# Performance work log

Hardware: AMD Instinct MI355X
Metric: run time of the kernel (lower is better)

## Reference

```python
import jax, jax.numpy as jnp
import numpy as np

B, N, DF = 8, 4096, 768
K1, K2, DS = 8, 2, 128
KVQ, H, ITERS = 128, 1, 3
DH = KVQ // H
EPS_SA = 1e-8
SCALE = DH ** -0.5


def layer_norm(x, g, b, eps=1e-5):
    m = jnp.mean(x, axis=-1, keepdims=True)
    v = jnp.var(x, axis=-1, keepdims=True)
    return (x - m) / jnp.sqrt(v + eps) * g + b


def gru_cell(x, h, Wih, Whh, bih, bhh):
    gi = x @ Wih.T + bih
    gh = h @ Whh.T + bhh
    ir, iz, inn = jnp.split(gi, 3, axis=-1)
    hr, hz, hn = jnp.split(gh, 3, axis=-1)
    r = jax.nn.sigmoid(ir + hr)
    z = jax.nn.sigmoid(iz + hz)
    n = jnp.tanh(inn + r * hn)
    return (1.0 - z) * n + z * h


def setup_inputs() -> dict:
    key = jax.random.key(0)
    ks = jax.random.split(key, 24)
    s = 0.02
    f32 = jnp.float32
    return {
        'tokens': jax.random.normal(ks[0], (B, N, DF), f32),
        'parent_slots': jax.random.normal(ks[1], (B, K1, DS), f32),
        'parent_masks': jax.random.uniform(ks[2], (B, K1, N), f32),
        'eps_noise': jax.random.normal(ks[3], (B, K1, K2, DS), f32),
        'ln_in_g': jnp.ones((DF,), f32), 'ln_in_b': jnp.zeros((DF,), f32),
        'ln_s_g': jnp.ones((DS,), f32), 'ln_s_b': jnp.zeros((DS,), f32),
        'Wq': jax.random.normal(ks[4], (KVQ, DS), f32) * s,
        'Wk': jax.random.normal(ks[5], (KVQ, DF), f32) * s,
        'Wv': jax.random.normal(ks[6], (KVQ, DF), f32) * s,
        'gru_Wih': jax.random.normal(ks[7], (3 * DS, KVQ), f32) * s,
        'gru_Whh': jax.random.normal(ks[8], (3 * DS, DS), f32) * s,
        'gru_bih': jnp.zeros((3 * DS,), f32),
        'gru_bhh': jnp.zeros((3 * DS,), f32),
        'mlp_ln_g': jnp.ones((DS,), f32), 'mlp_ln_b': jnp.zeros((DS,), f32),
        'mlp_W1': jax.random.normal(ks[9], (4 * DS, DS), f32) * s,
        'mlp_b1': jnp.zeros((4 * DS,), f32),
        'mlp_W2': jax.random.normal(ks[10], (DS, 4 * DS), f32) * s,
        'mlp_b2': jnp.zeros((DS,), f32),
    }


def reference(tokens, parent_slots, parent_masks, eps_noise,
              ln_in_g, ln_in_b, ln_s_g, ln_s_b, Wq, Wk, Wv,
              gru_Wih, gru_Whh, gru_bih, gru_bhh,
              mlp_ln_g, mlp_ln_b, mlp_W1, mlp_b1, mlp_W2, mlp_b2):
    BK = B * K1
    # parent-mask gating (all parents vectorized, folded into batch)
    denom = jnp.mean(parent_masks, axis=-1, keepdims=True)          # [B,K1,1]
    safe = (denom > 1e-6).astype(tokens.dtype)
    w_scaled = safe * (parent_masks / (denom + 1e-6)) + (1.0 - safe)  # [B,K1,N]
    tg = (tokens[:, None, :, :] * w_scaled[..., None]).reshape(BK, N, DF)
    slots = (parent_slots[:, :, None, :] + 0.01 * eps_noise).reshape(BK, K2, DS)

    inp = layer_norm(tg, ln_in_g, ln_in_b)
    k = (inp @ Wk.T).reshape(BK, N, H, DH)
    v = (inp @ Wv.T).reshape(BK, N, H, DH)

    attn_bw = None
    for _ in range(ITERS):
        slots_prev = slots
        sn = layer_norm(slots, ln_s_g, ln_s_b)
        q = (sn @ Wq.T).reshape(BK, K2, H, DH)
        dots = jnp.einsum('bihd,bjhd->bihj', q, k) * SCALE          # [BK,K2,H,N]
        attn = jax.nn.softmax(dots, axis=1) + EPS_SA                # softmax over slots
        attn_bw = attn
        attn_w = attn / jnp.sum(attn, axis=-1, keepdims=True)
        updates = jnp.einsum('bjhd,bihj->bihd', v, attn_w).reshape(BK * K2, KVQ)
        slots = gru_cell(updates, slots_prev.reshape(BK * K2, DS),
                         gru_Wih, gru_Whh, gru_bih, gru_bhh).reshape(BK, K2, DS)
        h = layer_norm(slots, mlp_ln_g, mlp_ln_b)
        slots = jax.nn.gelu(h @ mlp_W1.T + mlp_b1, approximate=False) @ mlp_W2.T + mlp_b2

    attn_out = jnp.mean(attn_bw, axis=2)                            # [BK,K2,N]
    child_objects = slots.reshape(B, K1 * K2, DS)
    child_gating = (attn_out.reshape(B, K1, K2, N) * parent_masks[:, :, None, :]).reshape(B, K1 * K2, N)
    return child_objects, child_gating
```

## Files before the change

kernel.cpp:

```cpp
#include <hip/hip_runtime.h>
#include <math.h>

#define SCALE_ 0.08838834764831843f

typedef __attribute__((ext_vector_type(8))) short bf16x8;
typedef __attribute__((ext_vector_type(4))) float f32x4;

static const size_t OFF_VAR   = 0;
static const size_t OFF_DENOM = 32768;
static const size_t OFF_GSUM  = 32832;
static const size_t OFF_BIAS  = 33088;
static const size_t OFF_QKB   = 33344;
static const size_t OFF_SSUM  = 33472;
static const size_t OFF_SLOTS = 33600;
static const size_t OFF_Q     = 49984;
static const size_t OFF_WQT   = 66368;
static const size_t OFF_WQBF  = 82752;
static const size_t OFF_WIHBF = 90944;
static const size_t OFF_WHHBF = 115520;
static const size_t OFF_W1BF  = 140096;
static const size_t OFF_WM2BF = 172864;
static const size_t OFF_WKVBF = 205632;
static const size_t OFF_UPART = 303936;
static const size_t OFF_KV    = 828224;

__device__ __forceinline__ float wred64(float v) {
#pragma unroll
  for (int off = 32; off > 0; off >>= 1) v += __shfl_xor(v, off, 64);
  return v;
}

__device__ __forceinline__ float2 bred128(float a, float b, float* red4, int t) {
  float ra = wred64(a), rb = wred64(b);
  int wid = t >> 6;
  if ((t & 63) == 0) { red4[wid] = ra; red4[2 + wid] = rb; }
  __syncthreads();
  float2 o; o.x = red4[0] + red4[1]; o.y = red4[2] + red4[3];
  __syncthreads();
  return o;
}

__device__ __forceinline__ unsigned short f2bf(float f) {
  unsigned u = __float_as_uint(f);
  unsigned r = (u + 0x7fffu + ((u >> 16) & 1u)) >> 16;
  return (unsigned short)r;
}

__device__ __forceinline__ unsigned pack2(float a, float b) {
  return (unsigned)f2bf(a) | ((unsigned)f2bf(b) << 16);
}

__global__ __launch_bounds__(64) void prep_w_k(
    const float* __restrict__ Wk, const float* __restrict__ Wv,
    const float* __restrict__ g, const float* __restrict__ bb,
    unsigned short* __restrict__ wkv, float* __restrict__ gsum,
    float* __restrict__ biasArr)
{
  int j = blockIdx.x, lane = threadIdx.x;
  const float* w = (j < 128) ? (Wk + (size_t)j*768) : (Wv + (size_t)(j-128)*768);
  float gs = 0.f, bs = 0.f;
#pragma unroll
  for (int s = 0; s < 12; ++s) {
    int dd = lane + s*64;
    float wv = w[dd], gv = g[dd];
    gs += gv*wv; bs += bb[dd]*wv;
    wkv[(size_t)j*768 + dd] = f2bf(wv*gv);
  }
  gs = wred64(gs); bs = wred64(bs);
  if (lane == 0) { gsum[j] = gs; biasArr[j] = bs; }
}

__global__ __launch_bounds__(256) void prep_bf_k(
    const float* __restrict__ Wq, const float* __restrict__ Wih,
    const float* __restrict__ Whh, const float* __restrict__ W1,
    const float* __restrict__ W2,
    float* __restrict__ WqT, unsigned short* __restrict__ Wqbf,
    unsigned short* __restrict__ Wihbf, unsigned short* __restrict__ Whhbf,
    unsigned short* __restrict__ W1bf, unsigned short* __restrict__ Wm2bf)
{
  int bi = blockIdx.x, t = threadIdx.x;
  if (bi < 64) {
    int idx = bi*256 + t;
    int r = idx >> 7, c = idx & 127;
    WqT[(size_t)c*128 + r] = Wq[idx];
    Wqbf[idx] = f2bf(Wq[idx]);
    return;
  }
  const float* src; unsigned short* dst; int idx;
  if (bi < 256)      { src = Wih; dst = Wihbf; idx = (bi-64)*256 + t; }
  else if (bi < 448) { src = Whh; dst = Whhbf; idx = (bi-256)*256 + t; }
  else if (bi < 704) { src = W1;  dst = W1bf;  idx = (bi-448)*256 + t; }
  else               { src = W2;  dst = Wm2bf; idx = (bi-704)*256 + t; }
  dst[idx] = f2bf(src[idx]);
}

__global__ __launch_bounds__(256) void denom_k(
    const float* __restrict__ pm, float* __restrict__ denomArr)
{
  __shared__ float red4[4];
  int bk = blockIdx.x, t = threadIdx.x;
  float s = 0.f;
#pragma unroll
  for (int k = 0; k < 16; ++k) s += pm[bk*4096 + t + k*256];
  s = wred64(s);
  if ((t & 63) == 0) red4[t >> 6] = s;
  __syncthreads();
  if (t == 0) denomArr[bk] = (red4[0]+red4[1]+red4[2]+red4[3])*(1.f/4096.f);
}

__global__ __launch_bounds__(256) void gemm_kv_k(
    const float* __restrict__ tokens, const unsigned short* __restrict__ wkv,
    const float* __restrict__ gsum, float* __restrict__ KV,
    float* __restrict__ varArr)
{
  __shared__ unsigned short As[128*64];
  __shared__ unsigned short Bs[128*64];
  int bi = blockIdx.x;
  int jb = bi & 1, rb = bi >> 1;
  int r0 = rb*128, j0 = jb*128;
  int t = threadIdx.x;
  int w = t >> 6, lane = t & 63;
  int j4 = t & 15, rowb = t >> 4;
  int m0w = (w >> 1)*64, n0w = (w & 1)*64;
  int lm = lane & 15, lq = lane >> 4;

  f32x4 acc[4][4];
#pragma unroll
  for (int a = 0; a < 4; ++a)
#pragma unroll
    for (int c = 0; c < 4; ++c) acc[a][c] = f32x4{0.f, 0.f, 0.f, 0.f};

  float s1[8], s2[8];
#pragma unroll
  for (int s = 0; s < 8; ++s) { s1[s] = 0.f; s2[s] = 0.f; }

  for (int k0 = 0; k0 < 768; k0 += 64) {
    __syncthreads();
#pragma unroll
    for (int s = 0; s < 4; ++s) {
      int row = w*32 + s*8;
      __builtin_amdgcn_global_load_lds(
        (const __attribute__((address_space(1))) void*)
          (wkv + (size_t)(j0 + row + (lane >> 3))*768 + k0 + (lane & 7)*8),
        (__attribute__((address_space(3))) void*)(&Bs[row*64]), 16, 0, 0);
    }
#pragma unroll
    for (int s = 0; s < 8; ++s) {
      int row = rowb + s*16;
      float4 x = *(const float4*)(tokens + (size_t)(r0 + row)*768 + k0 + j4*4);
      s1[s] += x.x + x.y + x.z + x.w;
      s2[s] += x.x*x.x + x.y*x.y + x.z*x.z + x.w*x.w;
      *(uint2*)(&As[row*64 + j4*4]) = make_uint2(pack2(x.x, x.y), pack2(x.z, x.w));
    }
    __syncthreads();
#pragma unroll
    for (int kk = 0; kk < 64; kk += 32) {
      bf16x8 af[4], bfr[4];
#pragma unroll
      for (int mt = 0; mt < 4; ++mt)
        af[mt] = *(const bf16x8*)(&As[(m0w + mt*16 + lm)*64 + kk + lq*8]);
#pragma unroll
      for (int nt = 0; nt < 4; ++nt)
        bfr[nt] = *(const bf16x8*)(&Bs[(n0w + nt*16 + lm)*64 + kk + lq*8]);
#pragma unroll
      for (int mt = 0; mt < 4; ++mt)
#pragma unroll
        for (int nt = 0; nt < 4; ++nt)
          acc[mt][nt] = __builtin_amdgcn_mfma_f32_16x16x32_bf16(
              af[mt], bfr[nt], acc[mt][nt], 0, 0, 0);
    }
  }
  __syncthreads();
  float* meanS = (float*)As;
#pragma unroll
  for (int s = 0; s < 8; ++s) {
#pragma unroll
    for (int m = 8; m >= 1; m >>= 1) {
      s1[s] += __shfl_xor(s1[s], m, 16);
      s2[s] += __shfl_xor(s2[s], m, 16);
    }
  }
  if (j4 == 0) {
#pragma unroll
    for (int s = 0; s < 8; ++s) {
      int row = rowb + s*16;
      float m = s1[s]*(1.f/768.f);
      meanS[row] = m;
      if (jb == 0) varArr[r0 + row] = s2[s]*(1.f/768.f) - m*m;
    }
  }
  __syncthreads();
#pragma unroll
  for (int nt = 0; nt < 4; ++nt) {
    int jg = j0 + n0w + nt*16 + lm;
    float gs = gsum[jg];
#pragma unroll
    for (int mt = 0; mt < 4; ++mt) {
#pragma unroll
      for (int reg = 0; reg < 4; ++reg) {
        int rl = m0w + mt*16 + lq*4 + reg;
        KV[(size_t)(r0 + rl)*256 + jg] = acc[mt][nt][reg] - meanS[rl]*gs;
      }
    }
  }
}

__global__ __launch_bounds__(128) void slots_init_q_k(
    const float* __restrict__ ps, const float* __restrict__ eps,
    const float* __restrict__ g_s, const float* __restrict__ b_s,
    const float* __restrict__ WqT, const float* __restrict__ biasArr,
    float* __restrict__ slots, float* __restrict__ qg, float* __restrict__ qkb,
    float* __restrict__ Ssum)
{
  __shared__ float sn[128];
  __shared__ float red4[4];
  int row = blockIdx.x, d = threadIdx.x, bk = row >> 1;
  float x = ps[bk*128 + d] + 0.01f*eps[row*128 + d];
  slots[row*128 + d] = x;
  float2 mv = bred128(x, x*x, red4, d);
  float m = mv.x*(1.f/128.f);
  float v = mv.y*(1.f/128.f) - m*m;
  sn[d] = (x - m)*rsqrtf(v + 1e-5f)*g_s[d] + b_s[d];
  __syncthreads();
  float qv = 0.f;
#pragma unroll 4
  for (int e = 0; e < 128; ++e) qv += sn[e]*WqT[e*128 + d];
  qg[row*128 + d] = qv;
  float2 qb = bred128(qv*biasArr[d], 0.f, red4, d);
  if (d == 0) { qkb[row] = qb.x; Ssum[row] = 0.f; }
}

__global__ __launch_bounds__(256) void attn_fused_k(
    const float* __restrict__ KV, const float* __restrict__ qg,
    const float* __restrict__ qkb, const float* __restrict__ varArr,
    const float* __restrict__ denomArr, const float* __restrict__ pm,
    float* __restrict__ Upart, float* __restrict__ Ssum,
    float* __restrict__ outG, int last)
{
  __shared__ float KVs[32*260];
  __shared__ float qs[2048];
  __shared__ float was[16*33];
  __shared__ float qkbs[16];
  int bi = blockIdx.x;
  int b = bi & 7, ch = bi >> 3;
  int t = threadIdx.x;
#pragma unroll
  for (int s = 0; s < 2; ++s)
    ((float4*)qs)[s*256 + t] = ((const float4*)(qg + b*2048))[s*256 + t];
  if (t < 16) qkbs[t] = qkb[b*16 + t];
  int p = t >> 5, nl = t & 31;
  int iu = t >> 4, dg = t & 15;
  int bk = b*8 + p;
  float den = denomArr[bk];
  float acc8[8];
#pragma unroll
  for (int j = 0; j < 8; ++j) acc8[j] = 0.f;
  float sA0 = 0.f, sA1 = 0.f;
  const float* q0 = qs + (p*2)*128;
  const float* q1 = q0 + 128;
  __syncthreads();
  float qb0 = qkbs[p*2], qb1 = qkbs[p*2 + 1];
  for (int sub = 0; sub < 4; ++sub) {
    int n0 = ch*128 + sub*32;
    if (sub) __syncthreads();
    {
      int nn = t >> 3;
      int jj = t & 7;
#pragma unroll
      for (int s = 0; s < 8; ++s) {
        int j4 = jj + s*8;
        *(float4*)&KVs[nn*260 + j4*4] =
          *(const float4*)&KV[((size_t)(b*4096 + n0 + nn))*256 + j4*4];
      }
    }
    __syncthreads();
    float d0 = 0.f, d1 = 0.f;
    const float* kr = KVs + nl*260;
#pragma unroll 8
    for (int j4 = 0; j4 < 32; ++j4) {
      float4 kv = *(const float4*)(kr + j4*4);
      float4 qa = *(const float4*)(q0 + j4*4);
      float4 qb = *(const float4*)(q1 + j4*4);
      d0 += kv.x*qa.x + kv.y*qa.y + kv.z*qa.z + kv.w*qa.w;
      d1 += kv.x*qb.x + kv.y*qb.y + kv.z*qb.z + kv.w*qb.w;
    }
    int n = n0 + nl;
    float pmv = pm[(size_t)bk*4096 + n];
    float c = (den > 1e-6f) ? (pmv/(den + 1e-6f)) : 1.f;
    float vv = varArr[b*4096 + n];
    float al = c*rsqrtf(c*c*vv + 1e-5f);
    float dd0 = SCALE_*(al*d0 + qb0);
    float dd1 = SCALE_*(al*d1 + qb1);
    float mx = fmaxf(dd0, dd1);
    float e0 = expf(dd0 - mx), e1 = expf(dd1 - mx);
    float inv = 1.f/(e0 + e1);
    float o0 = e0*inv + 1e-8f;
    float o1 = e1*inv + 1e-8f;
    sA0 += o0; sA1 += o1;
    was[(p*2)*33 + nl] = o0*al;
    was[(p*2 + 1)*33 + nl] = o1*al;
    if (last) {
      outG[((size_t)(bk*2))*4096 + n] = o0*pmv;
      outG[((size_t)(bk*2 + 1))*4096 + n] = o1*pmv;
    }
    __syncthreads();
    const float* vb = KVs + 128 + dg*8;
    const float* wr = was + iu*33;
#pragma unroll 8
    for (int nn = 0; nn < 32; ++nn) {
      float wv = wr[nn];
      float4 v0 = *(const float4*)(vb + nn*260);
      float4 v1 = *(const float4*)(vb + nn*260 + 4);
      acc8[0] += wv*v0.x; acc8[1] += wv*v0.y; acc8[2] += wv*v0.z; acc8[3] += wv*v0.w;
      acc8[4] += wv*v1.x; acc8[5] += wv*v1.y; acc8[6] += wv*v1.z; acc8[7] += wv*v1.w;
    }
  }
#pragma unroll
  for (int m = 16; m >= 1; m >>= 1) {
    sA0 += __shfl_xor(sA0, m, 32);
    sA1 += __shfl_xor(sA1, m, 32);
  }
  if (nl == 0) {
    atomicAdd(&Ssum[bk*2], sA0);
    atomicAdd(&Ssum[bk*2 + 1], sA1);
  }
  float* up = Upart + ((size_t)(bi*16 + iu))*128 + dg*8;
  *(float4*)up = make_float4(acc8[0], acc8[1], acc8[2], acc8[3]);
  *(float4*)(up + 4) = make_float4(acc8[4], acc8[5], acc8[6], acc8[7]);
}

__global__ __launch_bounds__(256, 1) void gru_mlp_q_k(
    const float* __restrict__ Upart, const float* __restrict__ Ssum,
    const float* __restrict__ biasArr,
    const unsigned short* __restrict__ Wihbf, const unsigned short* __restrict__ Whhbf,
    const float* __restrict__ bih, const float* __restrict__ bhh,
    const float* __restrict__ mlp_g, const float* __restrict__ mlp_b,
    const unsigned short* __restrict__ W1bf, const float* __restrict__ b1,
    const unsigned short* __restrict__ Wm2bf, const float* __restrict__ b2,
    const float* __restrict__ ln_s_g, const float* __restrict__ ln_s_b,
    const unsigned short* __restrict__ Wqbf,
    float* __restrict__ slots, float* __restrict__ qg, float* __restrict__ qkb,
    float* __restrict__ SsumW, float* __restrict__ outObj, int last)
{
  __shared__ unsigned short FXx[2048], FXh[2048], Fhn[2048], Fsn[2048];
  __shared__ unsigned short Ft1[8192];
  __shared__ float G_rz[16*256];
  __shared__ float G_in[16*128];
  __shared__ float G_hn[16*128];
  __shared__ float hs_[16*128];
  __shared__ float os_[16*128];
  __shared__ float qkbL[16];

  int blk = blockIdx.x;
  int R0 = blk*16;
  int t = threadIdx.x;
  int w = t >> 6, ln = t & 63;
  int lm = ln & 15, lq = ln >> 4;

  {
    int r = t >> 4, dseg = t & 15, ds8 = dseg*8;
    int R = R0 + r;
    float ua[8];
#pragma unroll
    for (int j = 0; j < 8; ++j) ua[j] = 0.f;
    const float* up = Upart + (size_t)R*128 + ds8;
#pragma unroll 4
    for (int ch = 0; ch < 32; ++ch) {
      float4 u0 = *(const float4*)(up + (size_t)ch*16384);
      float4 u1 = *(const float4*)(up + (size_t)ch*16384 + 4);
      ua[0]+=u0.x; ua[1]+=u0.y; ua[2]+=u0.z; ua[3]+=u0.w;
      ua[4]+=u1.x; ua[5]+=u1.y; ua[6]+=u1.z; ua[7]+=u1.w;
    }
    float Sv = 1.f/Ssum[R];
    float4 bv0 = *(const float4*)(biasArr + 128 + ds8);
    float4 bv1 = *(const float4*)(biasArr + 132 + ds8);
    float xv[8];
    xv[0]=ua[0]*Sv+bv0.x; xv[1]=ua[1]*Sv+bv0.y; xv[2]=ua[2]*Sv+bv0.z; xv[3]=ua[3]*Sv+bv0.w;
    xv[4]=ua[4]*Sv+bv1.x; xv[5]=ua[5]*Sv+bv1.y; xv[6]=ua[6]*Sv+bv1.z; xv[7]=ua[7]*Sv+bv1.w;
    float4 h0 = *(const float4*)(slots + (size_t)R*128 + ds8);
    float4 h1 = *(const float4*)(slots + (size_t)R*128 + ds8 + 4);
    *(float4*)(hs_ + r*128 + ds8) = h0;
    *(float4*)(hs_ + r*128 + ds8 + 4) = h1;
    int fa = ((dseg >> 2)*64 + (dseg & 3)*16 + r)*8;
    *(uint4*)&FXx[fa] = make_uint4(pack2(xv[0],xv[1]), pack2(xv[2],xv[3]),
                                   pack2(xv[4],xv[5]), pack2(xv[6],xv[7]));
    *(uint4*)&FXh[fa] = make_uint4(pack2(h0.x,h0.y), pack2(h0.z,h0.w),
                                   pack2(h1.x,h1.y), pack2(h1.z,h1.w));
    if (t < 16) qkbL[t] = 0.f;
  }
  __syncthreads();

  {
    bf16x8 ax[4], ah[4];
#pragma unroll
    for (int kc = 0; kc < 4; ++kc) {
      ax[kc] = *(const bf16x8*)(&FXx[(kc*64 + ln)*8]);
      ah[kc] = *(const bf16x8*)(&FXh[(kc*64 + ln)*8]);
    }
    if (w < 2) {
#pragma unroll
      for (int i = 0; i < 8; ++i) {
        int n0 = (w*8 + i)*16;
        f32x4 acc = f32x4{0.f,0.f,0.f,0.f};
#pragma unroll
        for (int kc = 0; kc < 4; ++kc) {
          bf16x8 bi_ = *(const bf16x8*)(&Wihbf[(size_t)(n0+lm)*128 + kc*32 + lq*8]);
          acc = __builtin_amdgcn_mfma_f32_16x16x32_bf16(ax[kc], bi_, acc, 0,0,0);
        }
#pragma unroll
        for (int kc = 0; kc < 4; ++kc) {
          bf16x8 bh_ = *(const bf16x8*)(&Whhbf[(size_t)(n0+lm)*128 + kc*32 + lq*8]);
          acc = __builtin_amdgcn_mfma_f32_16x16x32_bf16(ah[kc], bh_, acc, 0,0,0);
        }
#pragma unroll
        for (int reg = 0; reg < 4; ++reg)
          G_rz[(lq*4+reg)*256 + n0 + lm] = acc[reg];
      }
    } else if (w == 2) {
#pragma unroll
      for (int i = 0; i < 8; ++i) {
        int n0 = 256 + i*16;
        f32x4 acc = f32x4{0.f,0.f,0.f,0.f};
#pragma unroll
        for (int kc = 0; kc < 4; ++kc) {
          bf16x8 bi_ = *(const bf16x8*)(&Wihbf[(size_t)(n0+lm)*128 + kc*32 + lq*8]);
          acc = __builtin_amdgcn_mfma_f32_16x16x32_bf16(ax[kc], bi_, acc, 0,0,0);
        }
#pragma unroll
        for (int reg = 0; reg < 4; ++reg)
          G_in[(lq*4+reg)*128 + i*16 + lm] = acc[reg];
      }
    } else {
#pragma unroll
      for (int i = 0; i < 8; ++i) {
        int n0 = 256 + i*16;
        f32x4 acc = f32x4{0.f,0.f,0.f,0.f};
#pragma unroll
        for (int kc = 0; kc < 4; ++kc) {
          bf16x8 bh_ = *(const bf16x8*)(&Whhbf[(size_t)(n0+lm)*128 + kc*32 + lq*8]);
          acc = __builtin_amdgcn_mfma_f32_16x16x32_bf16(ah[kc], bh_, acc, 0,0,0);
        }
#pragma unroll
        for (int reg = 0; reg < 4; ++reg)
          G_hn[(lq*4+reg)*128 + i*16 + lm] = acc[reg];
      }
    }
  }
  __syncthreads();

  {
    int r = t >> 4, dseg = t & 15, ds8 = dseg*8;
    float hp[8];
    float s1 = 0.f, s2 = 0.f;
#pragma unroll
    for (int j = 0; j < 8; ++j) {
      int d = ds8 + j;
      float rg = G_rz[r*256 + d] + bih[d] + bhh[d];
      float zg = G_rz[r*256 + 128 + d] + bih[128+d] + bhh[128+d];
      float ing = G_in[r*128 + d] + bih[256+d];
      float hng = G_hn[r*128 + d] + bhh[256+d];
      float rv = 1.f/(1.f + expf(-rg));
      float zv = 1.f/(1.f + expf(-zg));
      float nv = tanhf(ing + rv*hng);
      float h0 = hs_[r*128 + d];
      float h = (1.f - zv)*nv + zv*h0;
      hp[j] = h;
      s1 += h; s2 += h*h;
    }
#pragma unroll
    for (int m = 8; m >= 1; m >>= 1) {
      s1 += __shfl_xor(s1, m, 16);
      s2 += __shfl_xor(s2, m, 16);
    }
    float mean = s1*(1.f/128.f);
    float var = s2*(1.f/128.f) - mean*mean;
    float rstd = rsqrtf(var + 1e-5f);
    float hv[8];
#pragma unroll
    for (int j = 0; j < 8; ++j) {
      int d = ds8 + j;
      hv[j] = (hp[j] - mean)*rstd*mlp_g[d] + mlp_b[d];
    }
    int fa = ((dseg >> 2)*64 + (dseg & 3)*16 + r)*8;
    *(uint4*)&Fhn[fa] = make_uint4(pack2(hv[0],hv[1]), pack2(hv[2],hv[3]),
                                   pack2(hv[4],hv[5]), pack2(hv[6],hv[7]));
  }
  __syncthreads();

  {
    bf16x8 af[4];
#pragma unroll
    for (int kc = 0; kc < 4; ++kc)
      af[kc] = *(const bf16x8*)(&Fhn[(kc*64 + ln)*8]);
#pragma unroll
    for (int i = 0; i < 8; ++i) {
      int n0 = (w*8 + i)*16;
      f32x4 acc = f32x4{0.f,0.f,0.f,0.f};
#pragma unroll
      for (int kc = 0; kc < 4; ++kc) {
        bf16x8 bw = *(const bf16x8*)(&W1bf[(size_t)(n0+lm)*128 + kc*32 + lq*8]);
        acc = __builtin_amdgcn_mfma_f32_16x16x32_bf16(af[kc], bw, acc, 0,0,0);
      }
      int kdim = n0 + lm;
      float bb = b1[kdim];
      int kc2 = kdim >> 5;
      int sub = (kdim >> 3) & 3;
      int jj = kdim & 7;
#pragma unroll
      for (int reg = 0; reg < 4; ++reg) {
        float v = acc[reg] + bb;
        float gel = 0.5f*v*(1.f + erff(v*0.70710678118654752f));
        Ft1[(kc2*64 + sub*16 + lq*4 + reg)*8 + jj] = f2bf(gel);
      }
    }
  }
  __syncthreads();

  {
#pragma unroll
    for (int i = 0; i < 2; ++i) {
      int n0 = w*32 + i*16;
      f32x4 acc = f32x4{0.f,0.f,0.f,0.f};
#pragma unroll
      for (int kc = 0; kc < 16; ++kc) {
        bf16x8 af = *(const bf16x8*)(&Ft1[(kc*64 + ln)*8]);
        bf16x8 bw = *(const bf16x8*)(&Wm2bf[(size_t)(n0+lm)*512 + kc*32 + lq*8]);
        acc = __builtin_amdgcn_mfma_f32_16x16x32_bf16(af, bw, acc, 0,0,0);
      }
      int n = n0 + lm;
      float bb = b2[n];
#pragma unroll
      for (int reg = 0; reg < 4; ++reg) {
        int row = lq*4 + reg;
        float o = acc[reg] + bb;
        slots[(size_t)(R0 + row)*128 + n] = o;
        os_[row*128 + n] = o;
        if (last) outObj[(size_t)(R0 + row)*128 + n] = o;
      }
    }
  }

  if (last) return;

  __syncthreads();
  {
    int r = t >> 4, dseg = t & 15, ds8 = dseg*8;
    float ov[8];
    float s1 = 0.f, s2 = 0.f;
#pragma unroll
    for (int j = 0; j < 8; ++j) {
      float o = os_[r*128 + ds8 + j];
      ov[j] = o; s1 += o; s2 += o*o;
    }
#pragma unroll
    for (int m = 8; m >= 1; m >>= 1) {
      s1 += __shfl_xor(s1, m, 16);
      s2 += __shfl_xor(s2, m, 16);
    }
    float mean = s1*(1.f/128.f);
    float var = s2*(1.f/128.f) - mean*mean;
    float rstd = rsqrtf(var + 1e-5f);
    float sv[8];
#pragma unroll
    for (int j = 0; j < 8; ++j) {
      int d = ds8 + j;
      sv[j] = (ov[j] - mean)*rstd*ln_s_g[d] + ln_s_b[d];
    }
    int fa = ((dseg >> 2)*64 + (dseg & 3)*16 + r)*8;
    *(uint4*)&Fsn[fa] = make_uint4(pack2(sv[0],sv[1]), pack2(sv[2],sv[3]),
                                   pack2(sv[4],sv[5]), pack2(sv[6],sv[7]));
  }
  __syncthreads();

  {
    bf16x8 af[4];
#pragma unroll
    for (int kc = 0; kc < 4; ++kc)
      af[kc] = *(const bf16x8*)(&Fsn[(kc*64 + ln)*8]);
    float pr[4] = {0.f, 0.f, 0.f, 0.f};
#pragma unroll
    for (int i = 0; i < 2; ++i) {
      int n0 = w*32 + i*16;
      f32x4 acc = f32x4{0.f,0.f,0.f,0.f};
#pragma unroll
      for (int kc = 0; kc < 4; ++kc) {
        bf16x8 bw = *(const bf16x8*)(&Wqbf[(size_t)(n0+lm)*128 + kc*32 + lq*8]);
        acc = __builtin_amdgcn_mfma_f32_16x16x32_bf16(af[kc], bw, acc, 0,0,0);
      }
      int n = n0 + lm;
      float bk_ = biasArr[n];
#pragma unroll
      for (int reg = 0; reg < 4; ++reg) {
        int row = lq*4 + reg;
        qg[(size_t)(R0 + row)*128 + n] = acc[reg];
        pr[reg] += acc[reg]*bk_;
      }
    }
#pragma unroll
    for (int reg = 0; reg < 4; ++reg) {
#pragma unroll
      for (int m = 8; m >= 1; m >>= 1) pr[reg] += __shfl_xor(pr[reg], m, 16);
    }
    if (lm == 0) {
#pragma unroll
      for (int reg = 0; reg < 4; ++reg)
        atomicAdd(&qkbL[lq*4 + reg], pr[reg]);
    }
  }
  __syncthreads();
  if (t < 16) {
    qkb[R0 + t] = qkbL[t];
    SsumW[R0 + t] = 0.f;
  }
}

extern "C" void kernel_launch(void* const* d_in, const int* in_sizes, int n_in,
                              void* d_out, int out_size, void* d_ws, size_t ws_size,
                              hipStream_t stream) {
  const float* tokens = (const float*)d_in[0];
  const float* pslots = (const float*)d_in[1];
  const float* pmasks = (const float*)d_in[2];
  const float* eps    = (const float*)d_in[3];
  const float* ln_in_g= (const float*)d_in[4];
  const float* ln_in_b= (const float*)d_in[5];
  const float* ln_s_g = (const float*)d_in[6];
  const float* ln_s_b = (const float*)d_in[7];
  const float* Wq     = (const float*)d_in[8];
  const float* Wk     = (const float*)d_in[9];
  const float* Wv     = (const float*)d_in[10];
  const float* Wih    = (const float*)d_in[11];
  const float* Whh    = (const float*)d_in[12];
  const float* bih    = (const float*)d_in[13];
  const float* bhh    = (const float*)d_in[14];
  const float* mlp_g  = (const float*)d_in[15];
  const float* mlp_b  = (const float*)d_in[16];
  const float* W1     = (const float*)d_in[17];
  const float* b1     = (const float*)d_in[18];
  const float* W2     = (const float*)d_in[19];
  const float* b2     = (const float*)d_in[20];
  float* ws  = (float*)d_ws;
  float* out = (float*)d_out;
  unsigned short* wkvbf = (unsigned short*)(ws + OFF_WKVBF);
  unsigned short* wqbf  = (unsigned short*)(ws + OFF_WQBF);
  unsigned short* wihbf = (unsigned short*)(ws + OFF_WIHBF);
  unsigned short* whhbf = (unsigned short*)(ws + OFF_WHHBF);
  unsigned short* w1bf  = (unsigned short*)(ws + OFF_W1BF);
  unsigned short* wm2bf = (unsigned short*)(ws + OFF_WM2BF);

  prep_w_k<<<256, 64, 0, stream>>>(Wk, Wv, ln_in_g, ln_in_b,
                                   wkvbf, ws + OFF_GSUM, ws + OFF_BIAS);
  prep_bf_k<<<960, 256, 0, stream>>>(Wq, Wih, Whh, W1, W2,
                                     ws + OFF_WQT, wqbf, wihbf, whhbf,
                                     w1bf, wm2bf);
  denom_k<<<64, 256, 0, stream>>>(pmasks, ws + OFF_DENOM);
  gemm_kv_k<<<512, 256, 0, stream>>>(tokens, wkvbf, ws + OFF_GSUM,
                                     ws + OFF_KV, ws + OFF_VAR);
  slots_init_q_k<<<128, 128, 0, stream>>>(pslots, eps, ln_s_g, ln_s_b,
                                          ws + OFF_WQT, ws + OFF_BIAS,
                                          ws + OFF_SLOTS, ws + OFF_Q,
                                          ws + OFF_QKB, ws + OFF_SSUM);
  for (int it = 0; it < 3; ++it) {
    int last = (it == 2);
    attn_fused_k<<<256, 256, 0, stream>>>(ws + OFF_KV, ws + OFF_Q, ws + OFF_QKB,
                                          ws + OFF_VAR, ws + OFF_DENOM, pmasks,
                                          ws + OFF_UPART, ws + OFF_SSUM,
                                          out + 16384, last);
    gru_mlp_q_k<<<8, 256, 0, stream>>>(ws + OFF_UPART, ws + OFF_SSUM,
                                       ws + OFF_BIAS, wihbf, whhbf, bih, bhh,
                                       mlp_g, mlp_b, w1bf, b1, wm2bf, b2,
                                       ln_s_g, ln_s_b, wqbf,
                                       ws + OFF_SLOTS, ws + OFF_Q, ws + OFF_QKB,
                                       ws + OFF_SSUM, out, last);
  }
}
```

Before: 380.9 us.

## Store K/V in bf16, swizzle GEMM LDS tiles, merge prep kernels, atomically reduce updates

The projected K/V intermediate is now written as bf16 and widened to fp32 in the attention kernel, which halves the traffic of the tensor that is re-read on every iteration. The KV GEMM is retiled to 64 rows by all 256 columns, with an XOR swizzle on both LDS tiles (the weight layout is pre-swizzled in prep) to avoid bank conflicts. The three prep kernels become one launch, and slot init with the Q projection now uses MFMA. Per-block partial updates are summed with atomics into a single buffer that is re-zeroed between iterations, replacing the 32-way partial reduction. The cost is lower K/V precision and atomic contention.

New measurement: 397.8 us. +4.4%, slower.

```diff
diff --git a/kernel.cpp b/kernel.cpp
--- a/kernel.cpp
+++ b/kernel.cpp
@@ -5,6 +5,7 @@
 
 typedef __attribute__((ext_vector_type(8))) short bf16x8;
 typedef __attribute__((ext_vector_type(4))) float f32x4;
+typedef __attribute__((ext_vector_type(8))) unsigned short u16x8;
 
 static const size_t OFF_VAR   = 0;
 static const size_t OFF_DENOM = 32768;
@@ -14,30 +15,19 @@
 static const size_t OFF_SSUM  = 33472;
 static const size_t OFF_SLOTS = 33600;
 static const size_t OFF_Q     = 49984;
-static const size_t OFF_WQT   = 66368;
+static const size_t OFF_U     = 66368;
 static const size_t OFF_WQBF  = 82752;
 static const size_t OFF_WIHBF = 90944;
 static const size_t OFF_WHHBF = 115520;
 static const size_t OFF_W1BF  = 140096;
 static const size_t OFF_WM2BF = 172864;
 static const size_t OFF_WKVBF = 205632;
-static const size_t OFF_UPART = 303936;
-static const size_t OFF_KV    = 828224;
+static const size_t OFF_KVB   = 303936;
 
 __device__ __forceinline__ float wred64(float v) {
 #pragma unroll
   for (int off = 32; off > 0; off >>= 1) v += __shfl_xor(v, off, 64);
   return v;
-}
-
-__device__ __forceinline__ float2 bred128(float a, float b, float* red4, int t) {
-  float ra = wred64(a), rb = wred64(b);
-  int wid = t >> 6;
-  if ((t & 63) == 0) { red4[wid] = ra; red4[2 + wid] = rb; }
-  __syncthreads();
-  float2 o; o.x = red4[0] + red4[1]; o.y = red4[2] + red4[3];
-  __syncthreads();
-  return o;
 }
 
 __device__ __forceinline__ unsigned short f2bf(float f) {
@@ -50,191 +40,245 @@
   return (unsigned)f2bf(a) | ((unsigned)f2bf(b) << 16);
 }
 
-__global__ __launch_bounds__(64) void prep_w_k(
+__device__ __forceinline__ float bf2f(unsigned short s) {
+  return __uint_as_float((unsigned)s << 16);
+}
+
+__global__ __launch_bounds__(256) void prep_all_k(
     const float* __restrict__ Wk, const float* __restrict__ Wv,
     const float* __restrict__ g, const float* __restrict__ bb,
-    unsigned short* __restrict__ wkv, float* __restrict__ gsum,
-    float* __restrict__ biasArr)
-{
-  int j = blockIdx.x, lane = threadIdx.x;
-  const float* w = (j < 128) ? (Wk + (size_t)j*768) : (Wv + (size_t)(j-128)*768);
-  float gs = 0.f, bs = 0.f;
-#pragma unroll
-  for (int s = 0; s < 12; ++s) {
-    int dd = lane + s*64;
-    float wv = w[dd], gv = g[dd];
-    gs += gv*wv; bs += bb[dd]*wv;
-    wkv[(size_t)j*768 + dd] = f2bf(wv*gv);
-  }
-  gs = wred64(gs); bs = wred64(bs);
-  if (lane == 0) { gsum[j] = gs; biasArr[j] = bs; }
-}
-
-__global__ __launch_bounds__(256) void prep_bf_k(
     const float* __restrict__ Wq, const float* __restrict__ Wih,
     const float* __restrict__ Whh, const float* __restrict__ W1,
-    const float* __restrict__ W2,
-    float* __restrict__ WqT, unsigned short* __restrict__ Wqbf,
-    unsigned short* __restrict__ Wihbf, unsigned short* __restrict__ Whhbf,
-    unsigned short* __restrict__ W1bf, unsigned short* __restrict__ Wm2bf)
+    const float* __restrict__ W2, const float* __restrict__ pm,
+    unsigned short* __restrict__ wkv, float* __restrict__ gsum,
+    float* __restrict__ biasArr,
+    unsigned short* __restrict__ Wqbf, unsigned short* __restrict__ Wihbf,
+    unsigned short* __restrict__ Whhbf, unsigned short* __restrict__ W1bf,
+    unsigned short* __restrict__ Wm2bf, float* __restrict__ denomArr)
 {
+  __shared__ float red4[4];
   int bi = blockIdx.x, t = threadIdx.x;
   if (bi < 64) {
-    int idx = bi*256 + t;
-    int r = idx >> 7, c = idx & 127;
-    WqT[(size_t)c*128 + r] = Wq[idx];
-    Wqbf[idx] = f2bf(Wq[idx]);
-    return;
-  }
-  const float* src; unsigned short* dst; int idx;
-  if (bi < 256)      { src = Wih; dst = Wihbf; idx = (bi-64)*256 + t; }
-  else if (bi < 448) { src = Whh; dst = Whhbf; idx = (bi-256)*256 + t; }
-  else if (bi < 704) { src = W1;  dst = W1bf;  idx = (bi-448)*256 + t; }
-  else               { src = W2;  dst = Wm2bf; idx = (bi-704)*256 + t; }
-  dst[idx] = f2bf(src[idx]);
-}
-
-__global__ __launch_bounds__(256) void denom_k(
-    const float* __restrict__ pm, float* __restrict__ denomArr)
-{
-  __shared__ float red4[4];
-  int bk = blockIdx.x, t = threadIdx.x;
-  float s = 0.f;
-#pragma unroll
-  for (int k = 0; k < 16; ++k) s += pm[bk*4096 + t + k*256];
-  s = wred64(s);
-  if ((t & 63) == 0) red4[t >> 6] = s;
-  __syncthreads();
-  if (t == 0) denomArr[bk] = (red4[0]+red4[1]+red4[2]+red4[3])*(1.f/4096.f);
+    int j = bi*4 + (t >> 6), lane = t & 63;
+    const float* w = (j < 128) ? (Wk + (size_t)j*768) : (Wv + (size_t)(j-128)*768);
+    float gs = 0.f, bs = 0.f;
+    int key = j & 7;
+#pragma unroll
+    for (int s = 0; s < 12; ++s) {
+      int dd = lane + s*64;
+      float wv = w[dd], gv = g[dd];
+      gs += gv*wv; bs += bb[dd]*wv;
+      int sw = (dd & ~63) | (((((dd >> 3) & 7) ^ key)) << 3) | (dd & 7);
+      wkv[(size_t)j*768 + sw] = f2bf(wv*gv);
+    }
+    gs = wred64(gs); bs = wred64(bs);
+    if (lane == 0) { gsum[j] = gs; biasArr[j] = bs; }
+  } else if (bi < 128) {
+    int idx = (bi-64)*256 + t;  Wqbf[idx]  = f2bf(Wq[idx]);
+  } else if (bi < 320) {
+    int idx = (bi-128)*256 + t; Wihbf[idx] = f2bf(Wih[idx]);
+  } else if (bi < 512) {
+    int idx = (bi-320)*256 + t; Whhbf[idx] = f2bf(Whh[idx]);
+  } else if (bi < 768) {
+    int idx = (bi-512)*256 + t; W1bf[idx]  = f2bf(W1[idx]);
+  } else if (bi < 1024) {
+    int idx = (bi-768)*256 + t; Wm2bf[idx] = f2bf(W2[idx]);
+  } else {
+    int bk = bi - 1024;
+    float s = 0.f;
+#pragma unroll
+    for (int k = 0; k < 16; ++k) s += pm[bk*4096 + t + k*256];
+    s = wred64(s);
+    if ((t & 63) == 0) red4[t >> 6] = s;
+    __syncthreads();
+    if (t == 0) denomArr[bk] = (red4[0]+red4[1]+red4[2]+red4[3])*(1.f/4096.f);
+  }
 }
 
 __global__ __launch_bounds__(256) void gemm_kv_k(
     const float* __restrict__ tokens, const unsigned short* __restrict__ wkv,
-    const float* __restrict__ gsum, float* __restrict__ KV,
+    const float* __restrict__ gsum, unsigned short* __restrict__ KVb,
     float* __restrict__ varArr)
 {
-  __shared__ unsigned short As[128*64];
-  __shared__ unsigned short Bs[128*64];
-  int bi = blockIdx.x;
-  int jb = bi & 1, rb = bi >> 1;
-  int r0 = rb*128, j0 = jb*128;
+  __shared__ unsigned short As[64*64];
+  __shared__ unsigned short Bs[256*64];
+  __shared__ float meanS[64];
+  int r0 = blockIdx.x*64;
   int t = threadIdx.x;
   int w = t >> 6, lane = t & 63;
-  int j4 = t & 15, rowb = t >> 4;
-  int m0w = (w >> 1)*64, n0w = (w & 1)*64;
   int lm = lane & 15, lq = lane >> 4;
-
-  f32x4 acc[4][4];
-#pragma unroll
-  for (int a = 0; a < 4; ++a)
-#pragma unroll
-    for (int c = 0; c < 4; ++c) acc[a][c] = f32x4{0.f, 0.f, 0.f, 0.f};
-
-  float s1[8], s2[8];
-#pragma unroll
-  for (int s = 0; s < 8; ++s) { s1[s] = 0.f; s2[s] = 0.f; }
+  int g16 = t >> 4, seg = t & 15;
+  int m0 = (w >> 1)*32, n0 = (w & 1)*128;
+
+  f32x4 acc[2][8];
+#pragma unroll
+  for (int a = 0; a < 2; ++a)
+#pragma unroll
+    for (int c = 0; c < 8; ++c) acc[a][c] = f32x4{0.f, 0.f, 0.f, 0.f};
+  float s1[4] = {0.f,0.f,0.f,0.f}, s2[4] = {0.f,0.f,0.f,0.f};
 
   for (int k0 = 0; k0 < 768; k0 += 64) {
     __syncthreads();
 #pragma unroll
-    for (int s = 0; s < 4; ++s) {
-      int row = w*32 + s*8;
+    for (int s = 0; s < 8; ++s) {
+      int row = w*64 + s*8;
       __builtin_amdgcn_global_load_lds(
         (const __attribute__((address_space(1))) void*)
-          (wkv + (size_t)(j0 + row + (lane >> 3))*768 + k0 + (lane & 7)*8),
+          (wkv + (size_t)(row + (lane >> 3))*768 + k0 + (lane & 7)*8),
         (__attribute__((address_space(3))) void*)(&Bs[row*64]), 16, 0, 0);
     }
 #pragma unroll
-    for (int s = 0; s < 8; ++s) {
-      int row = rowb + s*16;
-      float4 x = *(const float4*)(tokens + (size_t)(r0 + row)*768 + k0 + j4*4);
-      s1[s] += x.x + x.y + x.z + x.w;
-      s2[s] += x.x*x.x + x.y*x.y + x.z*x.z + x.w*x.w;
-      *(uint2*)(&As[row*64 + j4*4]) = make_uint2(pack2(x.x, x.y), pack2(x.z, x.w));
+    for (int p = 0; p < 4; ++p) {
+      int row = p*16 + g16;
+      float4 x = *(const float4*)(tokens + (size_t)(r0 + row)*768 + k0 + seg*4);
+      s1[p] += x.x + x.y + x.z + x.w;
+      s2[p] += x.x*x.x + x.y*x.y + x.z*x.z + x.w*x.w;
+      int off = row*64 + (((seg >> 1) ^ (row & 7)) << 3) + (seg & 1)*4;
+      *(uint2*)(&As[off]) = make_uint2(pack2(x.x, x.y), pack2(x.z, x.w));
     }
     __syncthreads();
 #pragma unroll
-    for (int kk = 0; kk < 64; kk += 32) {
-      bf16x8 af[4], bfr[4];
-#pragma unroll
-      for (int mt = 0; mt < 4; ++mt)
-        af[mt] = *(const bf16x8*)(&As[(m0w + mt*16 + lm)*64 + kk + lq*8]);
-#pragma unroll
-      for (int nt = 0; nt < 4; ++nt)
-        bfr[nt] = *(const bf16x8*)(&Bs[(n0w + nt*16 + lm)*64 + kk + lq*8]);
-#pragma unroll
-      for (int mt = 0; mt < 4; ++mt)
-#pragma unroll
-        for (int nt = 0; nt < 4; ++nt)
+    for (int kk8 = 0; kk8 < 8; kk8 += 4) {
+      bf16x8 af[2], bfr[8];
+#pragma unroll
+      for (int mt = 0; mt < 2; ++mt) {
+        int row = m0 + mt*16 + lm;
+        af[mt] = *(const bf16x8*)(&As[row*64 + (((kk8 + lq) ^ (row & 7)) << 3)]);
+      }
+#pragma unroll
+      for (int nt = 0; nt < 8; ++nt) {
+        int row = n0 + nt*16 + lm;
+        bfr[nt] = *(const bf16x8*)(&Bs[row*64 + (((kk8 + lq) ^ (row & 7)) << 3)]);
+      }
+#pragma unroll
+      for (int mt = 0; mt < 2; ++mt)
+#pragma unroll
+        for (int nt = 0; nt < 8; ++nt)
           acc[mt][nt] = __builtin_amdgcn_mfma_f32_16x16x32_bf16(
               af[mt], bfr[nt], acc[mt][nt], 0, 0, 0);
     }
   }
-  __syncthreads();
-  float* meanS = (float*)As;
-#pragma unroll
-  for (int s = 0; s < 8; ++s) {
+#pragma unroll
+  for (int p = 0; p < 4; ++p) {
 #pragma unroll
     for (int m = 8; m >= 1; m >>= 1) {
-      s1[s] += __shfl_xor(s1[s], m, 16);
-      s2[s] += __shfl_xor(s2[s], m, 16);
-    }
-  }
-  if (j4 == 0) {
-#pragma unroll
-    for (int s = 0; s < 8; ++s) {
-      int row = rowb + s*16;
-      float m = s1[s]*(1.f/768.f);
+      s1[p] += __shfl_xor(s1[p], m, 16);
+      s2[p] += __shfl_xor(s2[p], m, 16);
+    }
+  }
+  if (seg == 0) {
+#pragma unroll
+    for (int p = 0; p < 4; ++p) {
+      int row = p*16 + g16;
+      float m = s1[p]*(1.f/768.f);
       meanS[row] = m;
-      if (jb == 0) varArr[r0 + row] = s2[s]*(1.f/768.f) - m*m;
-    }
-  }
-  __syncthreads();
-#pragma unroll
-  for (int nt = 0; nt < 4; ++nt) {
-    int jg = j0 + n0w + nt*16 + lm;
+      varArr[r0 + row] = s2[p]*(1.f/768.f) - m*m;
+    }
+  }
+  __syncthreads();
+#pragma unroll
+  for (int nt = 0; nt < 8; ++nt) {
+    int jg = n0 + nt*16 + lm;
     float gs = gsum[jg];
 #pragma unroll
-    for (int mt = 0; mt < 4; ++mt) {
+    for (int mt = 0; mt < 2; ++mt) {
 #pragma unroll
       for (int reg = 0; reg < 4; ++reg) {
-        int rl = m0w + mt*16 + lq*4 + reg;
-        KV[(size_t)(r0 + rl)*256 + jg] = acc[mt][nt][reg] - meanS[rl]*gs;
-      }
-    }
-  }
-}
-
-__global__ __launch_bounds__(128) void slots_init_q_k(
+        int rl = m0 + mt*16 + lq*4 + reg;
+        KVb[(size_t)(r0 + rl)*256 + jg] = f2bf(acc[mt][nt][reg] - meanS[rl]*gs);
+      }
+    }
+  }
+}
+
+__global__ __launch_bounds__(256, 1) void slots_init_q_k(
     const float* __restrict__ ps, const float* __restrict__ eps,
     const float* __restrict__ g_s, const float* __restrict__ b_s,
-    const float* __restrict__ WqT, const float* __restrict__ biasArr,
+    const unsigned short* __restrict__ Wqbf, const float* __restrict__ biasArr,
     float* __restrict__ slots, float* __restrict__ qg, float* __restrict__ qkb,
-    float* __restrict__ Ssum)
+    float* __restrict__ Ssum, float* __restrict__ U)
 {
-  __shared__ float sn[128];
-  __shared__ float red4[4];
-  int row = blockIdx.x, d = threadIdx.x, bk = row >> 1;
-  float x = ps[bk*128 + d] + 0.01f*eps[row*128 + d];
-  slots[row*128 + d] = x;
-  float2 mv = bred128(x, x*x, red4, d);
-  float m = mv.x*(1.f/128.f);
-  float v = mv.y*(1.f/128.f) - m*m;
-  sn[d] = (x - m)*rsqrtf(v + 1e-5f)*g_s[d] + b_s[d];
-  __syncthreads();
-  float qv = 0.f;
-#pragma unroll 4
-  for (int e = 0; e < 128; ++e) qv += sn[e]*WqT[e*128 + d];
-  qg[row*128 + d] = qv;
-  float2 qb = bred128(qv*biasArr[d], 0.f, red4, d);
-  if (d == 0) { qkb[row] = qb.x; Ssum[row] = 0.f; }
+  __shared__ unsigned short Fsn[2048];
+  __shared__ float qkbL[16];
+  int R0 = blockIdx.x*16;
+  int t = threadIdx.x;
+  int w = t >> 6, ln = t & 63, lm = ln & 15, lq = ln >> 4;
+  if (t < 16) qkbL[t] = 0.f;
+  {
+    int r = t >> 4, dseg = t & 15, ds8 = dseg*8;
+    int row = R0 + r, bk = row >> 1;
+    float xv[8]; float s1 = 0.f, s2 = 0.f;
+#pragma unroll
+    for (int j = 0; j < 8; ++j) {
+      int d = ds8 + j;
+      float x = ps[bk*128 + d] + 0.01f*eps[row*128 + d];
+      slots[row*128 + d] = x;
+      U[row*128 + d] = 0.f;
+      xv[j] = x; s1 += x; s2 += x*x;
+    }
+#pragma unroll
+    for (int m = 8; m >= 1; m >>= 1) {
+      s1 += __shfl_xor(s1, m, 16);
+      s2 += __shfl_xor(s2, m, 16);
+    }
+    float mean = s1*(1.f/128.f);
+    float var = s2*(1.f/128.f) - mean*mean;
+    float rstd = rsqrtf(var + 1e-5f);
+    float sv[8];
+#pragma unroll
+    for (int j = 0; j < 8; ++j) {
+      int d = ds8 + j;
+      sv[j] = (xv[j] - mean)*rstd*g_s[d] + b_s[d];
+    }
+    int fa = ((dseg >> 2)*64 + (dseg & 3)*16 + r)*8;
+    *(uint4*)&Fsn[fa] = make_uint4(pack2(sv[0],sv[1]), pack2(sv[2],sv[3]),
+                                   pack2(sv[4],sv[5]), pack2(sv[6],sv[7]));
+  }
+  __syncthreads();
+  {
+    bf16x8 af[4];
+#pragma unroll
+    for (int kc = 0; kc < 4; ++kc)
+      af[kc] = *(const bf16x8*)(&Fsn[(kc*64 + ln)*8]);
+    float pr[4] = {0.f, 0.f, 0.f, 0.f};
+#pragma unroll
+    for (int i = 0; i < 2; ++i) {
+      int n0 = w*32 + i*16;
+      f32x4 acc = f32x4{0.f,0.f,0.f,0.f};
+#pragma unroll
+      for (int kc = 0; kc < 4; ++kc) {
+        bf16x8 bw = *(const bf16x8*)(&Wqbf[(size_t)(n0+lm)*128 + kc*32 + lq*8]);
+        acc = __builtin_amdgcn_mfma_f32_16x16x32_bf16(af[kc], bw, acc, 0,0,0);
+      }
+      int n = n0 + lm;
+      float bk_ = biasArr[n];
+#pragma unroll
+      for (int reg = 0; reg < 4; ++reg) {
+        int row = lq*4 + reg;
+        qg[(size_t)(R0 + row)*128 + n] = acc[reg];
+        pr[reg] += acc[reg]*bk_;
+      }
+    }
+#pragma unroll
+    for (int reg = 0; reg < 4; ++reg) {
+#pragma unroll
+      for (int m = 8; m >= 1; m >>= 1) pr[reg] += __shfl_xor(pr[reg], m, 16);
+    }
+    if (lm == 0) {
+#pragma unroll
+      for (int reg = 0; reg < 4; ++reg)
+        atomicAdd(&qkbL[lq*4 + reg], pr[reg]);
+    }
+  }
+  __syncthreads();
+  if (t < 16) { qkb[R0 + t] = qkbL[t]; Ssum[R0 + t] = 0.f; }
 }
 
 __global__ __launch_bounds__(256) void attn_fused_k(
-    const float* __restrict__ KV, const float* __restrict__ qg,
+    const unsigned short* __restrict__ KVb, const float* __restrict__ qg,
     const float* __restrict__ qkb, const float* __restrict__ varArr,
     const float* __restrict__ denomArr, const float* __restrict__ pm,
-    float* __restrict__ Upart, float* __restrict__ Ssum,
+    float* __restrict__ U, float* __restrict__ Ssum,
     float* __restrict__ outG, int last)
 {
   __shared__ float KVs[32*260];
@@ -264,13 +308,16 @@
     int n0 = ch*128 + sub*32;
     if (sub) __syncthreads();
     {
-      int nn = t >> 3;
-      int jj = t & 7;
-#pragma unroll
-      for (int s = 0; s < 8; ++s) {
-        int j4 = jj + s*8;
-        *(float4*)&KVs[nn*260 + j4*4] =
-          *(const float4*)&KV[((size_t)(b*4096 + n0 + nn))*256 + j4*4];
+      int nn = t >> 3, jj = t & 7;
+#pragma unroll
+      for (int s = 0; s < 4; ++s) {
+        int col8 = jj + s*8;
+        u16x8 kv8 = *(const u16x8*)&KVb[((size_t)(b*4096 + n0 + nn))*256 + col8*8];
+        float4 f0, f1;
+        f0.x = bf2f(kv8[0]); f0.y = bf2f(kv8[1]); f0.z = bf2f(kv8[2]); f0.w = bf2f(kv8[3]);
+        f1.x = bf2f(kv8[4]); f1.y = bf2f(kv8[5]); f1.z = bf2f(kv8[6]); f1.w = bf2f(kv8[7]);
+        *(float4*)&KVs[nn*260 + col8*8] = f0;
+        *(float4*)&KVs[nn*260 + col8*8 + 4] = f1;
       }
     }
     __syncthreads();
@@ -324,13 +371,13 @@
     atomicAdd(&Ssum[bk*2], sA0);
     atomicAdd(&Ssum[bk*2 + 1], sA1);
   }
-  float* up = Upart + ((size_t)(bi*16 + iu))*128 + dg*8;
-  *(float4*)up = make_float4(acc8[0], acc8[1], acc8[2], acc8[3]);
-  *(float4*)(up + 4) = make_float4(acc8[4], acc8[5], acc8[6], acc8[7]);
+  float* ur = U + (size_t)(b*16 + iu)*128 + dg*8;
+#pragma unroll
+  for (int j = 0; j < 8; ++j) atomicAdd(ur + j, acc8[j]);
 }
 
 __global__ __launch_bounds__(256, 1) void gru_mlp_q_k(
-    const float* __restrict__ Upart, const float* __restrict__ Ssum,
+    const float* __restrict__ Uin, const float* __restrict__ Ssum,
     const float* __restrict__ biasArr,
     const unsigned short* __restrict__ Wihbf, const unsigned short* __restrict__ Whhbf,
     const float* __restrict__ bih, const float* __restrict__ bhh,
@@ -340,7 +387,8 @@
     const float* __restrict__ ln_s_g, const float* __restrict__ ln_s_b,
     const unsigned short* __restrict__ Wqbf,
     float* __restrict__ slots, float* __restrict__ qg, float* __restrict__ qkb,
-    float* __restrict__ SsumW, float* __restrict__ outObj, int last)
+    float* __restrict__ SsumW, float* __restrict__ Uw,
+    float* __restrict__ outObj, int last)
 {
   __shared__ unsigned short FXx[2048], FXh[2048], Fhn[2048], Fsn[2048];
   __shared__ unsigned short Ft1[8192];
@@ -351,8 +399,7 @@
   __shared__ float os_[16*128];
   __shared__ float qkbL[16];
 
-  int blk = blockIdx.x;
-  int R0 = blk*16;
+  int R0 = blockIdx.x*16;
   int t = threadIdx.x;
   int w = t >> 6, ln = t & 63;
   int lm = ln & 15, lq = ln >> 4;
@@ -360,23 +407,19 @@
   {
     int r = t >> 4, dseg = t & 15, ds8 = dseg*8;
     int R = R0 + r;
-    float ua[8];
-#pragma unroll
-    for (int j = 0; j < 8; ++j) ua[j] = 0.f;
-    const float* up = Upart + (size_t)R*128 + ds8;
-#pragma unroll 4
-    for (int ch = 0; ch < 32; ++ch) {
-      float4 u0 = *(const float4*)(up + (size_t)ch*16384);
-      float4 u1 = *(const float4*)(up + (size_t)ch*16384 + 4);
-      ua[0]+=u0.x; ua[1]+=u0.y; ua[2]+=u0.z; ua[3]+=u0.w;
-      ua[4]+=u1.x; ua[5]+=u1.y; ua[6]+=u1.z; ua[7]+=u1.w;
-    }
+    const float* up = Uin + (size_t)R*128 + ds8;
+    float4 u0 = *(const float4*)(up);
+    float4 u1 = *(const float4*)(up + 4);
     float Sv = 1.f/Ssum[R];
     float4 bv0 = *(const float4*)(biasArr + 128 + ds8);
     float4 bv1 = *(const float4*)(biasArr + 132 + ds8);
     float xv[8];
-    xv[0]=ua[0]*Sv+bv0.x; xv[1]=ua[1]*Sv+bv0.y; xv[2]=ua[2]*Sv+bv0.z; xv[3]=ua[3]*Sv+bv0.w;
-    xv[4]=ua[4]*Sv+bv1.x; xv[5]=ua[5]*Sv+bv1.y; xv[6]=ua[6]*Sv+bv1.z; xv[7]=ua[7]*Sv+bv1.w;
+    xv[0]=u0.x*Sv+bv0.x; xv[1]=u0.y*Sv+bv0.y; xv[2]=u0.z*Sv+bv0.z; xv[3]=u0.w*Sv+bv0.w;
+    xv[4]=u1.x*Sv+bv1.x; xv[5]=u1.y*Sv+bv1.y; xv[6]=u1.z*Sv+bv1.z; xv[7]=u1.w*Sv+bv1.w;
+    if (!last) {
+      *(float4*)(Uw + (size_t)R*128 + ds8) = make_float4(0.f,0.f,0.f,0.f);
+      *(float4*)(Uw + (size_t)R*128 + ds8 + 4) = make_float4(0.f,0.f,0.f,0.f);
+    }
     float4 h0 = *(const float4*)(slots + (size_t)R*128 + ds8);
     float4 h1 = *(const float4*)(slots + (size_t)R*128 + ds8 + 4);
     *(float4*)(hs_ + r*128 + ds8) = h0;
@@ -646,30 +689,31 @@
   unsigned short* whhbf = (unsigned short*)(ws + OFF_WHHBF);
   unsigned short* w1bf  = (unsigned short*)(ws + OFF_W1BF);
   unsigned short* wm2bf = (unsigned short*)(ws + OFF_WM2BF);
-
-  prep_w_k<<<256, 64, 0, stream>>>(Wk, Wv, ln_in_g, ln_in_b,
-                                   wkvbf, ws + OFF_GSUM, ws + OFF_BIAS);
-  prep_bf_k<<<960, 256, 0, stream>>>(Wq, Wih, Whh, W1, W2,
-                                     ws + OFF_WQT, wqbf, wihbf, whhbf,
-                                     w1bf, wm2bf);
-  denom_k<<<64, 256, 0, stream>>>(pmasks, ws + OFF_DENOM);
+  unsigned short* kvb   = (unsigned short*)(ws + OFF_KVB);
+
+  prep_all_k<<<1088, 256, 0, stream>>>(Wk, Wv, ln_in_g, ln_in_b,
+                                       Wq, Wih, Whh, W1, W2, pmasks,
+                                       wkvbf, ws + OFF_GSUM, ws + OFF_BIAS,
+                                       wqbf, wihbf, whhbf, w1bf, wm2bf,
+                                       ws + OFF_DENOM);
   gemm_kv_k<<<512, 256, 0, stream>>>(tokens, wkvbf, ws + OFF_GSUM,
-                                     ws + OFF_KV, ws + OFF_VAR);
-  slots_init_q_k<<<128, 128, 0, stream>>>(pslots, eps, ln_s_g, ln_s_b,
-                                          ws + OFF_WQT, ws + OFF_BIAS,
-                                          ws + OFF_SLOTS, ws + OFF_Q,
-                                          ws + OFF_QKB, ws + OFF_SSUM);
+                                     kvb, ws + OFF_VAR);
+  slots_init_q_k<<<8, 256, 0, stream>>>(pslots, eps, ln_s_g, ln_s_b,
+                                        wqbf, ws + OFF_BIAS,
+                                        ws + OFF_SLOTS, ws + OFF_Q,
+                                        ws + OFF_QKB, ws + OFF_SSUM,
+                                        ws + OFF_U);
   for (int it = 0; it < 3; ++it) {
     int last = (it == 2);
-    attn_fused_k<<<256, 256, 0, stream>>>(ws + OFF_KV, ws + OFF_Q, ws + OFF_QKB,
+    attn_fused_k<<<256, 256, 0, stream>>>(kvb, ws + OFF_Q, ws + OFF_QKB,
                                           ws + OFF_VAR, ws + OFF_DENOM, pmasks,
-                                          ws + OFF_UPART, ws + OFF_SSUM,
+                                          ws + OFF_U, ws + OFF_SSUM,
                                           out + 16384, last);
-    gru_mlp_q_k<<<8, 256, 0, stream>>>(ws + OFF_UPART, ws + OFF_SSUM,
+    gru_mlp_q_k<<<8, 256, 0, stream>>>(ws + OFF_U, ws + OFF_SSUM,
                                        ws + OFF_BIAS, wihbf, whhbf, bih, bhh,
                                        mlp_g, mlp_b, w1bf, b1, wm2bf, b2,
                                        ln_s_g, ln_s_b, wqbf,
                                        ws + OFF_SLOTS, ws + OFF_Q, ws + OFF_QKB,
-                                       ws + OFF_SSUM, out, last);
-  }
-}
+                                       ws + OFF_SSUM, ws + OFF_U, out, last);
+  }
+}
```
